# Kernel optimization log

Measured on AMD Instinct MI355X. Metric: run time of the kernel, lower is better.

## Reference

```python
import jax, jax.numpy as jnp
import numpy as np

NV, NS = 100000, 50000
DG, DS, H, OUT = 5, 6, 64, 8
EVV, EH, EIN, ESS = 1_000_000, 1_000_000, 500_000, 1_000_000


def _segsum(data, idx, n):
    return jax.ops.segment_sum(data, idx, num_segments=n)


def _edge_index(key, e, n_src, n_dst):
    k1, k2 = jax.random.split(key)
    return jnp.stack([
        jax.random.randint(k1, (e,), 0, n_src),
        jax.random.randint(k2, (e,), 0, n_dst),
    ]).astype(jnp.int64)


def setup_inputs() -> dict:
    key = jax.random.key(0)
    ks = jax.random.split(key, 16)
    s = 0.1
    inp = {
        "game_x": jax.random.normal(ks[0], (NV, DG), jnp.float32),
        "state_x": jax.random.normal(ks[1], (NS, DS), jnp.float32),
        "edge_index_v_v": _edge_index(ks[2], EVV, NV, NV),
        "edge_index_history_v_s": _edge_index(ks[3], EH, NV, NS),
        "edge_attr_history_v_s": jax.random.uniform(ks[4], (EH,), jnp.float32),
        "edge_index_in_v_s": _edge_index(ks[5], EIN, NV, NS),
        "edge_index_s_s": _edge_index(ks[6], ESS, NS, NS),
        # TAGConv(5, H, K=2): K+1 bias-free linears + bias
        "tag1_W": jax.random.normal(ks[7], (3, DG, H), jnp.float32) * s,
        "tag1_b": jnp.zeros((H,), jnp.float32),
        # TAGConv(H, H, K=3)
        "tag2_W": jax.random.normal(ks[8], (4, H, H), jnp.float32) * s,
        "tag2_b": jnp.zeros((H,), jnp.float32),
        # GraphConv((-1,-1), H): lin_rel (bias) + lin_root (no bias)
        "gc_W_rel": jax.random.normal(ks[9], (H, H), jnp.float32) * s,
        "gc_b": jnp.zeros((H,), jnp.float32),
        "gc_W_root": jax.random.normal(ks[10], (DS, H), jnp.float32) * s,
        # SAGEConv((-1,-1), H): lin_l (bias) + lin_r (no bias), mean aggr
        "sage_W_l": jax.random.normal(ks[11], (H, H), jnp.float32) * s,
        "sage_b_l": jnp.zeros((H,), jnp.float32),
        "sage_W_r": jax.random.normal(ks[12], (H, H), jnp.float32) * s,
        "lin_W": jax.random.normal(ks[13], (H, OUT), jnp.float32) * s,
        "lin_b": jnp.zeros((OUT,), jnp.float32),
    }
    return inp


def _tag_conv(x, edge_index, W, b):
    # TAGConv with gcn_norm (no self-loops): out = sum_k lin_k(A_hat^k x) + b
    n = x.shape[0]
    src, dst = edge_index[0], edge_index[1]
    deg = _segsum(jnp.ones(src.shape[0], x.dtype), dst, n)
    dinv = jnp.where(deg > 0, jax.lax.rsqrt(jnp.maximum(deg, 1e-12)), 0.0)
    norm = dinv[src] * dinv[dst]  # [E]
    out = x @ W[0]
    h = x
    for k in range(1, W.shape[0]):  # fixed, small K
        h = _segsum(h[src] * norm[:, None], dst, n)
        out = out + h @ W[k]
    return out + b


def _forward(game_x, state_x, edge_attr_history_v_s,
             tag1_W, tag1_b, tag2_W, tag2_b,
             gc_W_rel, gc_b, gc_W_root,
             sage_W_l, sage_b_l, sage_W_r, lin_W, lin_b,
             edge_index_v_v, edge_index_history_v_s,
             edge_index_in_v_s, edge_index_s_s):
    ns = state_x.shape[0]
    gx = jax.nn.relu(_tag_conv(game_x, edge_index_v_v, tag1_W, tag1_b))
    # GraphConv bipartite with edge weights: lin_rel(sum w*x_j) + lin_root(x_dst)
    src, dst = edge_index_history_v_s[0], edge_index_history_v_s[1]
    agg = _segsum(gx[src] * edge_attr_history_v_s[:, None], dst, ns)
    sx = jax.nn.relu(agg @ gc_W_rel + gc_b + state_x @ gc_W_root)
    # SAGEConv bipartite, mean aggr: lin_l(mean x_j) + lin_r(x_dst)
    src, dst = edge_index_in_v_s[0], edge_index_in_v_s[1]
    ssum = _segsum(gx[src], dst, ns)
    cnt = _segsum(jnp.ones(src.shape[0], gx.dtype), dst, ns)
    mean = ssum / jnp.maximum(cnt, 1.0)[:, None]
    sx = jax.nn.relu(mean @ sage_W_l + sage_b_l + sx @ sage_W_r)
    sx = jax.nn.relu(_tag_conv(sx, edge_index_s_s, tag2_W, tag2_b))
    return sx @ lin_W + lin_b


def reference(game_x, state_x, edge_index_v_v, edge_index_history_v_s,
              edge_attr_history_v_s, edge_index_in_v_s, edge_index_s_s,
              tag1_W, tag1_b, tag2_W, tag2_b, gc_W_rel, gc_b, gc_W_root,
              sage_W_l, sage_b_l, sage_W_r, lin_W, lin_b):
    return _forward(game_x, state_x, edge_attr_history_v_s,
                    tag1_W, tag1_b, tag2_W, tag2_b,
                    gc_W_rel, gc_b, gc_W_root,
                    sage_W_l, sage_b_l, sage_W_r, lin_W, lin_b,
                    edge_index_v_v, edge_index_history_v_s,
                    edge_index_in_v_s, edge_index_s_s)
```

## Files before the change

### kernel.cpp

```cpp
#include <hip/hip_runtime.h>

#define BLK 256
#define ACH 4096

__device__ __forceinline__ float bcast(float v, int l) {
    return __int_as_float(__builtin_amdgcn_readlane(__float_as_int(v), l));
}
__device__ __forceinline__ unsigned short f2bf(float f) {
    unsigned u = __float_as_uint(f);
    return (unsigned short)((u + 0x7FFFu + ((u >> 16) & 1u)) >> 16);
}
__device__ __forceinline__ float bf2f(unsigned short b) {
    return __uint_as_float(((unsigned)b) << 16);
}

typedef __attribute__((ext_vector_type(8))) short bf16x8;
typedef __attribute__((ext_vector_type(4))) float f32x4;

__device__ __forceinline__ void split8s(const float* p, float s, bf16x8& h, bf16x8& l) {
    #pragma unroll
    for (int j = 0; j < 8; j++) {
        float v = p[j] * s;
        unsigned short hb = f2bf(v);
        h[j] = (short)hb;
        l[j] = (short)f2bf(v - bf2f(hb));
    }
}
__device__ __forceinline__ void loadWsplit(const float* W, int kbase, int col,
                                           bf16x8& h, bf16x8& l) {
    #pragma unroll
    for (int j = 0; j < 8; j++) {
        float v = W[(size_t)(kbase + j) * 64 + col];
        unsigned short hb = f2bf(v);
        h[j] = (short)hb;
        l[j] = (short)f2bf(v - bf2f(hb));
    }
}


__global__ void k_binA1(const int* __restrict__ vd, const int* __restrict__ hd,
                        const int* __restrict__ id_, const int* __restrict__ sd,
                        int* __restrict__ Tv, int* __restrict__ Th,
                        int* __restrict__ Ti, int* __restrict__ Ts,
                        int ncv, int nch, int nci, int ncs,
                        int nbv_, int nbs_, int Ev, int Eh, int Ei, int Es) {
    __shared__ int cnt[512];
    int blk = blockIdx.x, t = threadIdx.x;
    const int* dd; int* T; int c, nc, nb, E, sf;
    if (blk < ncv)                 { dd = vd;  T = Tv; c = blk;               nc = ncv; nb = nbv_; E = Ev; sf = 8; }
    else if (blk < ncv + nch)      { dd = hd;  T = Th; c = blk - ncv;         nc = nch; nb = nbs_; E = Eh; sf = 7; }
    else if (blk < ncv + nch + nci){ dd = id_; T = Ti; c = blk - ncv - nch;   nc = nci; nb = nbs_; E = Ei; sf = 7; }
    else                           { dd = sd;  T = Ts; c = blk - ncv - nch - nci; nc = ncs; nb = nbs_; E = Es; sf = 7; }
    cnt[t] = 0; cnt[t + 256] = 0;
    __syncthreads();
    int p0 = c * ACH, p1 = min(E, p0 + ACH);
    for (int p = p0 + t; p < p1; p += 256) atomicAdd(&cnt[dd[p] >> sf], 1);
    __syncthreads();
    for (int b = t; b < nb; b += 256) T[(size_t)b * nc + c] = cnt[b];
}

__global__ void k_sb2(int* __restrict__ T, int* __restrict__ bsum,
                      int L0, int L1, int L2, int L3,
                      int nB0, int nB1, int nB2, int nB3) {
    __shared__ int sh[256];
    int blk = blockIdx.x;
    int lb, off, L;
    if (blk < nB0)                  { lb = blk;                 off = 0;            L = L0; }
    else if (blk < nB0 + nB1)       { lb = blk - nB0;           off = L0;           L = L1; }
    else if (blk < nB0 + nB1 + nB2) { lb = blk - nB0 - nB1;     off = L0 + L1;      L = L2; }
    else                            { lb = blk - nB0 - nB1 - nB2; off = L0 + L1 + L2; L = L3; }
    int i = lb * 256 + threadIdx.x;
    int v = (i < L) ? T[off + i] : 0;
    sh[threadIdx.x] = v; __syncthreads();
    for (int o2 = 1; o2 < 256; o2 <<= 1) {
        int tmp = (threadIdx.x >= o2) ? sh[threadIdx.x - o2] : 0;
        __syncthreads();
        sh[threadIdx.x] += tmp; __syncthreads();
    }
    if (i < L) T[off + i] = sh[threadIdx.x] - v;
    if (threadIdx.x == 255) bsum[blk] = sh[255];
}

__global__ void k_st2(int* __restrict__ bsum, int nB0, int nB1, int nB2, int nB3) {
    __shared__ int sh[1024];
    int g = blockIdx.x;
    int off = (g == 0) ? 0 : (g == 1) ? nB0 : (g == 2) ? nB0 + nB1 : nB0 + nB1 + nB2;
    int nb  = (g == 0) ? nB0 : (g == 1) ? nB1 : (g == 2) ? nB2 : nB3;
    int tid = threadIdx.x;
    int v = (tid < nb) ? bsum[off + tid] : 0;
    sh[tid] = v; __syncthreads();
    for (int o2 = 1; o2 < 1024; o2 <<= 1) {
        int t = (tid >= o2) ? sh[tid - o2] : 0;
        __syncthreads();
        sh[tid] += t; __syncthreads();
    }
    if (tid < nb) bsum[off + tid] = sh[tid] - v;
}

__global__ void k_sa2(int* __restrict__ T, const int* __restrict__ bsum,
                      int L0, int L1, int L2, int L3,
                      int nB0, int nB1, int nB2, int nB3) {
    int blk = blockIdx.x;
    int lb, off, L;
    if (blk < nB0)                  { lb = blk;                 off = 0;            L = L0; }
    else if (blk < nB0 + nB1)       { lb = blk - nB0;           off = L0;           L = L1; }
    else if (blk < nB0 + nB1 + nB2) { lb = blk - nB0 - nB1;     off = L0 + L1;      L = L2; }
    else                            { lb = blk - nB0 - nB1 - nB2; off = L0 + L1 + L2; L = L3; }
    int i = lb * 256 + threadIdx.x;
    if (i < L) T[off + i] += bsum[blk];
}

__global__ __launch_bounds__(512)
void k_binA2a(const int* __restrict__ vs, const int* __restrict__ vd,
              const int* __restrict__ is_, const int* __restrict__ id_,
              const int* __restrict__ ss_, const int* __restrict__ sd,
              const int* __restrict__ Tv, const int* __restrict__ Ti,
              const int* __restrict__ Ts,
              unsigned* __restrict__ vvbin, unsigned* __restrict__ inbin,
              unsigned* __restrict__ ssbin,
              int ncv, int nci, int ncs, int nbv_, int nbs_,
              int Ev, int Ei, int Es) {
    __shared__ int gbase[512], lscan[512], lcur[512];
    __shared__ unsigned sval[ACH];
    __shared__ int sdst[ACH];
    int blk = blockIdx.x, t = threadIdx.x;
    const int *srcp, *dstp, *T; unsigned* bin; int c, nc, nb, E, sf;
    if (blk < ncv)            { srcp = vs;  dstp = vd;  T = Tv; bin = vvbin; c = blk;             nc = ncv; nb = nbv_; E = Ev; sf = 8; }
    else if (blk < ncv + nci) { srcp = is_; dstp = id_; T = Ti; bin = inbin; c = blk - ncv;       nc = nci; nb = nbs_; E = Ei; sf = 7; }
    else                      { srcp = ss_; dstp = sd;  T = Ts; bin = ssbin; c = blk - ncv - nci; nc = ncs; nb = nbs_; E = Es; sf = 7; }
    int msk = (1 << sf) - 1;
    int p0 = c * ACH, p1 = min(E, p0 + ACH);
    if (t < nb) gbase[t] = T[(size_t)t * nc + c];
    lcur[t] = 0;
    int myS[8], myD[8];
    #pragma unroll
    for (int i = 0; i < 8; i++) {
        int p = p0 + t + i * 512;
        if (p < p1) { myS[i] = srcp[p]; myD[i] = dstp[p]; }
        else myD[i] = -1;
    }
    __syncthreads();
    #pragma unroll
    for (int i = 0; i < 8; i++)
        if (myD[i] >= 0) atomicAdd(&lcur[myD[i] >> sf], 1);
    __syncthreads();
    int v = lcur[t];
    lscan[t] = v;
    __syncthreads();
    for (int off = 1; off < 512; off <<= 1) {
        int tmp = (t >= off) ? lscan[t - off] : 0;
        __syncthreads();
        lscan[t] += tmp;
        __syncthreads();
    }
    int excl = lscan[t] - v;
    __syncthreads();
    lscan[t] = excl;
    lcur[t] = 0;
    __syncthreads();
    #pragma unroll
    for (int i = 0; i < 8; i++) {
        if (myD[i] < 0) continue;
        int b = myD[i] >> sf;
        int r = atomicAdd(&lcur[b], 1);
        int pos = lscan[b] + r;
        sval[pos] = ((unsigned)myS[i] << sf) | (unsigned)(myD[i] & msk);
        sdst[pos] = gbase[b] + r;
    }
    __syncthreads();
    int cntE = p1 - p0;
    for (int q = t; q < cntE; q += 512) bin[sdst[q]] = sval[q];
}

__global__ __launch_bounds__(512)
void k_binA2h(const int* __restrict__ hs, const int* __restrict__ hd,
              const float* __restrict__ hw, const int* __restrict__ Th,
              int2* __restrict__ hbin, int nch, int nbs_, int Eh) {
    __shared__ int gbase[512], lscan[512], lcur[512];
    __shared__ unsigned sval[ACH];
    __shared__ int sdst[ACH];
    __shared__ float swt[ACH];
    int c = blockIdx.x, t = threadIdx.x;
    const int sf = 7, msk = 127;
    int p0 = c * ACH, p1 = min(Eh, p0 + ACH);
    if (t < nbs_) gbase[t] = Th[(size_t)t * nch + c];
    lcur[t] = 0;
    int myS[8], myD[8]; float myW[8];
    #pragma unroll
    for (int i = 0; i < 8; i++) {
        int p = p0 + t + i * 512;
        if (p < p1) { myS[i] = hs[p]; myD[i] = hd[p]; myW[i] = hw[p]; }
        else myD[i] = -1;
    }
    __syncthreads();
    #pragma unroll
    for (int i = 0; i < 8; i++)
        if (myD[i] >= 0) atomicAdd(&lcur[myD[i] >> sf], 1);
    __syncthreads();
    int v = lcur[t];
    lscan[t] = v;
    __syncthreads();
    for (int off = 1; off < 512; off <<= 1) {
        int tmp = (t >= off) ? lscan[t - off] : 0;
        __syncthreads();
        lscan[t] += tmp;
        __syncthreads();
    }
    int excl = lscan[t] - v;
    __syncthreads();
    lscan[t] = excl;
    lcur[t] = 0;
    __syncthreads();
    #pragma unroll
    for (int i = 0; i < 8; i++) {
        if (myD[i] < 0) continue;
        int b = myD[i] >> sf;
        int r = atomicAdd(&lcur[b], 1);
        int pos = lscan[b] + r;
        sval[pos] = ((unsigned)myS[i] << sf) | (unsigned)(myD[i] & msk);
        sdst[pos] = gbase[b] + r;
        swt[pos] = myW[i];
    }
    __syncthreads();
    int cntE = p1 - p0;
    for (int q = t; q < cntE; q += 512)
        hbin[sdst[q]] = make_int2((int)sval[q], __float_as_int(swt[q]));
}

__global__ void k_binB(const unsigned* __restrict__ vvbin, const int2* __restrict__ hbin,
                       const unsigned* __restrict__ inbin, const unsigned* __restrict__ ssbin,
                       const int* __restrict__ Tv, const int* __restrict__ Th,
                       const int* __restrict__ Ti, const int* __restrict__ Ts,
                       int* __restrict__ rv, int* __restrict__ rh,
                       int* __restrict__ ri, int* __restrict__ rs,
                       float* __restrict__ dinv_v, float* __restrict__ dinv_s,
                       int* __restrict__ vvsrc, int2* __restrict__ hsw,
                       int* __restrict__ insrc, int* __restrict__ sssrc,
                       int ncv, int nch, int nci, int ncs,
                       int nbv_, int nbs_, int nv, int ns,
                       int Ev, int Eh, int Ei, int Es) {
    __shared__ int cnt[256]; __shared__ int pre[256]; __shared__ int cur[256];
    int blk = blockIdx.x, t = threadIdx.x;
    int g, b, nb, nc, sf, n, E; const int* T; int* rp;
    if (blk < nbv_)                 { g = 0; b = blk;                 nb = nbv_; nc = ncv; sf = 8; n = nv; E = Ev; T = Tv; rp = rv; }
    else if (blk < nbv_ + nbs_)     { g = 1; b = blk - nbv_;          nb = nbs_; nc = nch; sf = 7; n = ns; E = Eh; T = Th; rp = rh; }
    else if (blk < nbv_ + 2 * nbs_) { g = 2; b = blk - nbv_ - nbs_;   nb = nbs_; nc = nci; sf = 7; n = ns; E = Ei; T = Ti; rp = ri; }
    else                            { g = 3; b = blk - nbv_ - 2 * nbs_; nb = nbs_; nc = ncs; sf = 7; n = ns; E = Es; T = Ts; rp = rs; }
    int W = 1 << sf, msk = W - 1;
    int e0 = T[(size_t)b * nc];
    int e1 = (b + 1 < nb) ? T[(size_t)(b + 1) * nc] : E;
    cnt[t] = 0; __syncthreads();
    for (int p = e0 + t; p < e1; p += 256) {
        unsigned pk = (g == 1) ? (unsigned)hbin[p].x
                    : (g == 0) ? vvbin[p] : (g == 2) ? inbin[p] : ssbin[p];
        atomicAdd(&cnt[pk & msk], 1);
    }
    __syncthreads();
    int v = cnt[t];
    pre[t] = v; __syncthreads();
    for (int o2 = 1; o2 < 256; o2 <<= 1) {
        int tmp = (t >= o2) ? pre[t - o2] : 0;
        __syncthreads();
        pre[t] += tmp; __syncthreads();
    }
    int excl = pre[t] - v;
    int d = b * W + t;
    if (t < W && d < n) {
        rp[d] = e0 + excl;
        if (g == 0)      dinv_v[d] = v > 0 ? rsqrtf((float)v) : 0.f;
        else if (g == 3) dinv_s[d] = v > 0 ? rsqrtf((float)v) : 0.f;
    }
    cur[t] = e0 + excl;
    __syncthreads();
    for (int p = e0 + t; p < e1; p += 256) {
        if (g == 1) {
            int2 r = hbin[p];
            unsigned pk = (unsigned)r.x;
            int pos = atomicAdd(&cur[pk & msk], 1);
            hsw[pos] = make_int2((int)(pk >> sf), r.y);
        } else {
            unsigned pk = (g == 0) ? vvbin[p] : (g == 2) ? inbin[p] : ssbin[p];
            int pos = atomicAdd(&cur[pk & msk], 1);
            int sv = (int)(pk >> sf);
            if (g == 0)      vvsrc[pos] = sv;
            else if (g == 2) insrc[pos] = sv;
            else             sssrc[pos] = sv;
        }
    }
    if (b == 0 && t == 0) rp[n] = E;
}


__global__ void k_gather5(const float* __restrict__ x, const int* __restrict__ rowptr,
                          const int* __restrict__ csr_src, const float* __restrict__ dinv,
                          float* __restrict__ out, int n) {
    int d = blockIdx.x * blockDim.x + threadIdx.x;
    if (d >= n) return;
    int b = rowptr[d], e = rowptr[d + 1];
    float dd = dinv[d];
    float a0 = 0, a1 = 0, a2 = 0, a3 = 0, a4 = 0;
    int p = b;
    for (; p + 4 <= e; p += 4) {
        int s0 = csr_src[p], s1 = csr_src[p+1], s2 = csr_src[p+2], s3 = csr_src[p+3];
        const float* x0 = x + (size_t)s0 * 5;
        const float* x1 = x + (size_t)s1 * 5;
        const float* x2 = x + (size_t)s2 * 5;
        const float* x3 = x + (size_t)s3 * 5;
        float w0 = dd * dinv[s0], w1 = dd * dinv[s1], w2 = dd * dinv[s2], w3 = dd * dinv[s3];
        a0 += x0[0]*w0 + x1[0]*w1 + x2[0]*w2 + x3[0]*w3;
        a1 += x0[1]*w0 + x1[1]*w1 + x2[1]*w2 + x3[1]*w3;
        a2 += x0[2]*w0 + x1[2]*w1 + x2[2]*w2 + x3[2]*w3;
        a3 += x0[3]*w0 + x1[3]*w1 + x2[3]*w2 + x3[3]*w3;
        a4 += x0[4]*w0 + x1[4]*w1 + x2[4]*w2 + x3[4]*w3;
    }
    for (; p < e; p++) {
        int s = csr_src[p];
        float w = dd * dinv[s];
        const float* xp = x + (size_t)s * 5;
        a0 += xp[0]*w; a1 += xp[1]*w; a2 += xp[2]*w; a3 += xp[3]*w; a4 += xp[4]*w;
    }
    float* op = out + (size_t)d * 5;
    op[0] = a0; op[1] = a1; op[2] = a2; op[3] = a3; op[4] = a4;
}

template<int MODE, bool OUTBF>
__global__ void k_gather64(const unsigned short* __restrict__ xbf, const int* __restrict__ rowptr,
                           const int* __restrict__ csr_src, const int2* __restrict__ csr_sw,
                           const float* __restrict__ dinv, void* __restrict__ outp, int n) {
    int wid = (int)(((long long)blockIdx.x * blockDim.x + threadIdx.x) >> 6);
    if (wid >= n) return;
    int lane = threadIdx.x & 63;
    int g = lane >> 4, q = lane & 15;
    int b = rowptr[wid], e = rowptr[wid + 1];
    float dd = (MODE == 2) ? dinv[wid] : 0.f;
    float4 acc = make_float4(0.f, 0.f, 0.f, 0.f);
    int p = b + g;
    for (; p + 12 < e; p += 16) {
        int s0, s1, s2, s3;
        float w0 = 1.f, w1 = 1.f, w2 = 1.f, w3 = 1.f;
        if (MODE == 1) {
            int2 e0 = csr_sw[p], e1 = csr_sw[p+4], e2 = csr_sw[p+8], e3 = csr_sw[p+12];
            s0 = e0.x; w0 = __int_as_float(e0.y);
            s1 = e1.x; w1 = __int_as_float(e1.y);
            s2 = e2.x; w2 = __int_as_float(e2.y);
            s3 = e3.x; w3 = __int_as_float(e3.y);
        } else {
            s0 = csr_src[p]; s1 = csr_src[p+4]; s2 = csr_src[p+8]; s3 = csr_src[p+12];
            if (MODE == 2) {
                w0 = dd * dinv[s0]; w1 = dd * dinv[s1];
                w2 = dd * dinv[s2]; w3 = dd * dinv[s3];
            }
        }
        ushort4 u0 = ((const ushort4*)(xbf + (size_t)s0 * 64))[q];
        ushort4 u1 = ((const ushort4*)(xbf + (size_t)s1 * 64))[q];
        ushort4 u2 = ((const ushort4*)(xbf + (size_t)s2 * 64))[q];
        ushort4 u3 = ((const ushort4*)(xbf + (size_t)s3 * 64))[q];
        acc.x += bf2f(u0.x)*w0 + bf2f(u1.x)*w1 + bf2f(u2.x)*w2 + bf2f(u3.x)*w3;
        acc.y += bf2f(u0.y)*w0 + bf2f(u1.y)*w1 + bf2f(u2.y)*w2 + bf2f(u3.y)*w3;
        acc.z += bf2f(u0.z)*w0 + bf2f(u1.z)*w1 + bf2f(u2.z)*w2 + bf2f(u3.z)*w3;
        acc.w += bf2f(u0.w)*w0 + bf2f(u1.w)*w1 + bf2f(u2.w)*w2 + bf2f(u3.w)*w3;
    }
    for (; p < e; p += 4) {
        int s; float w = 1.f;
        if (MODE == 1) { int2 e0 = csr_sw[p]; s = e0.x; w = __int_as_float(e0.y); }
        else { s = csr_src[p]; if (MODE == 2) w = dd * dinv[s]; }
        ushort4 u = ((const ushort4*)(xbf + (size_t)s * 64))[q];
        acc.x += bf2f(u.x)*w; acc.y += bf2f(u.y)*w;
        acc.z += bf2f(u.z)*w; acc.w += bf2f(u.w)*w;
    }
    #pragma unroll
    for (int off = 16; off < 64; off <<= 1) {
        acc.x += __shfl_xor(acc.x, off, 64);
        acc.y += __shfl_xor(acc.y, off, 64);
        acc.z += __shfl_xor(acc.z, off, 64);
        acc.w += __shfl_xor(acc.w, off, 64);
    }
    if (g == 0) {
        if (OUTBF) {
            ushort4 ov;
            ov.x = f2bf(acc.x); ov.y = f2bf(acc.y); ov.z = f2bf(acc.z); ov.w = f2bf(acc.w);
            ((ushort4*)outp)[(size_t)wid * 16 + q] = ov;
        } else {
            ((float4*)outp)[(size_t)wid * 16 + q] = acc;
        }
    }
}


template<bool INIT>
__global__ __launch_bounds__(256)
void k_mm_mf(const unsigned short* __restrict__ xbf, const float* __restrict__ W,
             const float* __restrict__ bias, float* __restrict__ out, int n) {
    int wv = (int)(((long long)blockIdx.x * blockDim.x + threadIdx.x) >> 6);
    int lane = threadIdx.x & 63;
    int r0 = wv * 32;
    if (r0 >= n) return;
    int lm = lane & 15, g = lane >> 4;
    bf16x8 a[2][2];
    #pragma unroll
    for (int mt = 0; mt < 2; mt++) {
        int row = r0 + mt * 16 + lm; if (row >= n) row = n - 1;
        #pragma unroll
        for (int kh = 0; kh < 2; kh++)
            a[mt][kh] = *(const bf16x8*)(xbf + (size_t)row * 64 + kh * 32 + g * 8);
    }
    #pragma unroll
    for (int nt = 0; nt < 4; nt++) {
        int col = nt * 16 + lm;
        bf16x8 bh[2], blo[2];
        #pragma unroll
        for (int kh = 0; kh < 2; kh++) loadWsplit(W, kh * 32 + g * 8, col, bh[kh], blo[kh]);
        #pragma unroll
        for (int mt = 0; mt < 2; mt++) {
            f32x4 acc = {0.f, 0.f, 0.f, 0.f};
            #pragma unroll
            for (int kh = 0; kh < 2; kh++) {
                acc = __builtin_amdgcn_mfma_f32_16x16x32_bf16(a[mt][kh], bh[kh],  acc, 0, 0, 0);
                acc = __builtin_amdgcn_mfma_f32_16x16x32_bf16(a[mt][kh], blo[kh], acc, 0, 0, 0);
            }
            #pragma unroll
            for (int r = 0; r < 4; r++) {
                int row = r0 + mt * 16 + g * 4 + r;
                if (row < n) {
                    float base = INIT ? bias[col] : out[(size_t)row * 64 + col];
                    out[(size_t)row * 64 + col] = base + acc[r];
                }
            }
        }
    }
}

__global__ __launch_bounds__(256)
void k_sage_mf(const float* __restrict__ ssum, const int* __restrict__ rp,
               const float* __restrict__ sx, const float* __restrict__ Wl,
               const float* __restrict__ Wr, const float* __restrict__ bl,
               unsigned short* __restrict__ out, int n) {
    int wv = (int)(((long long)blockIdx.x * blockDim.x + threadIdx.x) >> 6);
    int lane = threadIdx.x & 63;
    int r0 = wv * 32;
    if (r0 >= n) return;
    int lm = lane & 15, g = lane >> 4;
    bf16x8 axh[2][2], axl[2][2], ayh[2][2], ayl[2][2];
    #pragma unroll
    for (int mt = 0; mt < 2; mt++) {
        int row = r0 + mt * 16 + lm; if (row >= n) row = n - 1;
        float cnt = (float)(rp[row + 1] - rp[row]);
        float rs = 1.f / fmaxf(cnt, 1.f);
        #pragma unroll
        for (int kh = 0; kh < 2; kh++) {
            split8s(ssum + (size_t)row * 64 + kh * 32 + g * 8, rs,  axh[mt][kh], axl[mt][kh]);
            split8s(sx   + (size_t)row * 64 + kh * 32 + g * 8, 1.f, ayh[mt][kh], ayl[mt][kh]);
        }
    }
    #pragma unroll
    for (int nt = 0; nt < 4; nt++) {
        int col = nt * 16 + lm;
        bf16x8 blh[2], bll[2], brh[2], brl[2];
        #pragma unroll
        for (int kh = 0; kh < 2; kh++) {
            loadWsplit(Wl, kh * 32 + g * 8, col, blh[kh], bll[kh]);
            loadWsplit(Wr, kh * 32 + g * 8, col, brh[kh], brl[kh]);
        }
        #pragma unroll
        for (int mt = 0; mt < 2; mt++) {
            f32x4 acc = {0.f, 0.f, 0.f, 0.f};
            #pragma unroll
            for (int kh = 0; kh < 2; kh++) {
                acc = __builtin_amdgcn_mfma_f32_16x16x32_bf16(axh[mt][kh], blh[kh], acc, 0, 0, 0);
                acc = __builtin_amdgcn_mfma_f32_16x16x32_bf16(axl[mt][kh], blh[kh], acc, 0, 0, 0);
                acc = __builtin_amdgcn_mfma_f32_16x16x32_bf16(axh[mt][kh], bll[kh], acc, 0, 0, 0);
                acc = __builtin_amdgcn_mfma_f32_16x16x32_bf16(ayh[mt][kh], brh[kh], acc, 0, 0, 0);
                acc = __builtin_amdgcn_mfma_f32_16x16x32_bf16(ayl[mt][kh], brh[kh], acc, 0, 0, 0);
                acc = __builtin_amdgcn_mfma_f32_16x16x32_bf16(ayh[mt][kh], brl[kh], acc, 0, 0, 0);
            }
            #pragma unroll
            for (int r = 0; r < 4; r++) {
                int row = r0 + mt * 16 + g * 4 + r;
                if (row < n)
                    out[(size_t)row * 64 + col] = f2bf(fmaxf(bl[col] + acc[r], 0.f));
            }
        }
    }
}

__global__ __launch_bounds__(256)
void k_gc_mf(const float* __restrict__ agg, const float* __restrict__ st,
             const float* __restrict__ Wrel, const float* __restrict__ Wroot,
             const float* __restrict__ b, float* __restrict__ out, int n) {
    int wv = (int)(((long long)blockIdx.x * blockDim.x + threadIdx.x) >> 6);
    int lane = threadIdx.x & 63;
    int r0 = wv * 32;
    if (r0 >= n) return;
    int lm = lane & 15, g = lane >> 4;
    bf16x8 axh[2][2], axl[2][2], arh[2], arl[2];
    #pragma unroll
    for (int mt = 0; mt < 2; mt++) {
        int row = r0 + mt * 16 + lm; if (row >= n) row = n - 1;
        #pragma unroll
        for (int kh = 0; kh < 2; kh++)
            split8s(agg + (size_t)row * 64 + kh * 32 + g * 8, 1.f, axh[mt][kh], axl[mt][kh]);
        #pragma unroll
        for (int j = 0; j < 8; j++) {
            int k = g * 8 + j;
            float v = (k < 6) ? st[(size_t)row * 6 + k] : 0.f;
            unsigned short hb = f2bf(v);
            arh[mt][j] = (short)hb;
            arl[mt][j] = (short)f2bf(v - bf2f(hb));
        }
    }
    #pragma unroll
    for (int nt = 0; nt < 4; nt++) {
        int col = nt * 16 + lm;
        bf16x8 bh[2], blo[2], brh, brl;
        #pragma unroll
        for (int kh = 0; kh < 2; kh++) loadWsplit(Wrel, kh * 32 + g * 8, col, bh[kh], blo[kh]);
        #pragma unroll
        for (int j = 0; j < 8; j++) {
            int k = g * 8 + j;
            float v = (k < 6) ? Wroot[(size_t)k * 64 + col] : 0.f;
            unsigned short hb = f2bf(v);
            brh[j] = (short)hb;
            brl[j] = (short)f2bf(v - bf2f(hb));
        }
        #pragma unroll
        for (int mt = 0; mt < 2; mt++) {
            f32x4 acc = {0.f, 0.f, 0.f, 0.f};
            #pragma unroll
            for (int kh = 0; kh < 2; kh++) {
                acc = __builtin_amdgcn_mfma_f32_16x16x32_bf16(axh[mt][kh], bh[kh],  acc, 0, 0, 0);
                acc = __builtin_amdgcn_mfma_f32_16x16x32_bf16(axl[mt][kh], bh[kh],  acc, 0, 0, 0);
                acc = __builtin_amdgcn_mfma_f32_16x16x32_bf16(axh[mt][kh], blo[kh], acc, 0, 0, 0);
            }
            acc = __builtin_amdgcn_mfma_f32_16x16x32_bf16(arh[mt], brh, acc, 0, 0, 0);
            acc = __builtin_amdgcn_mfma_f32_16x16x32_bf16(arl[mt], brh, acc, 0, 0, 0);
            acc = __builtin_amdgcn_mfma_f32_16x16x32_bf16(arh[mt], brl, acc, 0, 0, 0);
            #pragma unroll
            for (int r = 0; r < 4; r++) {
                int row = r0 + mt * 16 + g * 4 + r;
                if (row < n)
                    out[(size_t)row * 64 + col] = fmaxf(b[col] + acc[r], 0.f);
            }
        }
    }
}

__global__ __launch_bounds__(256, 4)
void k_tag1_w(const float* __restrict__ x, const float* __restrict__ h1,
              const float* __restrict__ h2, const float* __restrict__ W,
              const float* __restrict__ b, unsigned short* __restrict__ out, int n) {
    int wv = (int)(((long long)blockIdx.x * blockDim.x + threadIdx.x) >> 6);
    int lane = threadIdx.x & 63;
    int i0 = wv * 4;
    if (i0 >= n) return;
    float v[4], acc[4];
    #pragma unroll
    for (int r = 0; r < 4; r++) {
        int i = (i0 + r < n) ? i0 + r : n - 1;
        float t = 0.f;
        if (lane < 5)                     t = x [(size_t)i * 5 + lane];
        else if (lane >= 8 && lane < 13)  t = h1[(size_t)i * 5 + lane - 8];
        else if (lane >= 16 && lane < 21) t = h2[(size_t)i * 5 + lane - 16];
        v[r] = t;
        acc[r] = b[lane];
    }
    #pragma unroll
    for (int m = 0; m < 3; m++) {
        #pragma unroll
        for (int k = 0; k < 5; k++) {
            float wk = W[(m * 5 + k) * 64 + lane];
            #pragma unroll
            for (int r = 0; r < 4; r++) acc[r] += bcast(v[r], m * 8 + k) * wk;
        }
    }
    #pragma unroll
    for (int r = 0; r < 4; r++)
        if (i0 + r < n) out[(size_t)(i0 + r) * 64 + lane] = f2bf(fmaxf(acc[r], 0.f));
}

__global__ void k_final(const float* __restrict__ x, const float* __restrict__ W,
                        const float* __restrict__ b, float* __restrict__ out, int n) {
    int t = blockIdx.x * blockDim.x + threadIdx.x;
    if (t >= n * 8) return;
    int i = t >> 3, o = t & 7;
    float acc = b[o];
    #pragma unroll 8
    for (int k = 0; k < 64; k++) acc += fmaxf(x[i * 64 + k], 0.f) * W[k * 8 + o];
    out[t] = acc;
}

static inline unsigned gblk(long long n) { return (unsigned)((n + BLK - 1) / BLK); }
static inline unsigned gwv4(long long n) { return gblk(((n + 3) / 4) * 64); }
static inline unsigned gw32(long long n) { return gblk(((n + 31) / 32) * 64); }

extern "C" void kernel_launch(void* const* d_in, const int* in_sizes, int n_in,
                              void* d_out, int out_size, void* d_ws, size_t ws_size,
                              hipStream_t stream) {
    const float* game_x  = (const float*)d_in[0];
    const float* state_x = (const float*)d_in[1];
    const int*   ei_vv   = (const int*)d_in[2];
    const int*   ei_h    = (const int*)d_in[3];
    const float* ea_h    = (const float*)d_in[4];
    const int*   ei_in   = (const int*)d_in[5];
    const int*   ei_ss   = (const int*)d_in[6];
    const float* tag1_W  = (const float*)d_in[7];
    const float* tag1_b  = (const float*)d_in[8];
    const float* tag2_W  = (const float*)d_in[9];
    const float* tag2_b  = (const float*)d_in[10];
    const float* gc_Wrel = (const float*)d_in[11];
    const float* gc_b    = (const float*)d_in[12];
    const float* gc_Wroot= (const float*)d_in[13];
    const float* sage_Wl = (const float*)d_in[14];
    const float* sage_bl = (const float*)d_in[15];
    const float* sage_Wr = (const float*)d_in[16];
    const float* lin_W   = (const float*)d_in[17];
    const float* lin_b   = (const float*)d_in[18];

    const int NV  = in_sizes[0] / 5;
    const int NS  = in_sizes[1] / 6;
    const int EVV = in_sizes[2] / 2;
    const int EH  = in_sizes[3] / 2;
    const int EIN = in_sizes[5] / 2;
    const int ESS = in_sizes[6] / 2;

    const int *vv_s = ei_vv,  *vv_d = ei_vv + EVV;
    const int *h_s  = ei_h,   *h_d  = ei_h  + EH;
    const int *in_s = ei_in,  *in_d = ei_in + EIN;
    const int *ss_s = ei_ss,  *ss_d = ei_ss + ESS;

    const int ncv = (EVV + ACH - 1) / ACH;
    const int nch = (EH  + ACH - 1) / ACH;
    const int nci = (EIN + ACH - 1) / ACH;
    const int ncs = (ESS + ACH - 1) / ACH;
    const int nbv_ = (NV + 255) >> 8;
    const int nbs_ = (NS + 127) >> 7;
    const int Lv = nbv_ * ncv, Lh = nbs_ * nch, Li = nbs_ * nci, Ls = nbs_ * ncs;
    const int nB0 = (Lv + 255) / 256, nB1 = (Lh + 255) / 256,
              nB2 = (Li + 255) / 256, nB3 = (Ls + 255) / 256;

    float* wsf = (float*)d_ws;
    size_t o = 0;
    unsigned short* gx_bf = (unsigned short*)(wsf + o);
    float* sx3 = wsf + o; o += (size_t)NV * 32;
    float* B1 = wsf + o; o += (size_t)NS * 64;
    float* B2 = wsf + o; o += (size_t)NS * 64;
    float* B4 = wsf + o; o += (size_t)NS * 32;
    int*  vvsrc = (int*)(wsf + o); o += (size_t)EVV;
    int*  sssrc = (int*)(wsf + o); o += (size_t)ESS;
    int*  insrc = (int*)(wsf + o); o += (size_t)EIN;
    int2* hsw   = (int2*)(wsf + o); o += (size_t)EH * 2;
    int* T_all = (int*)(wsf + o); o += (size_t)(Lv + Lh + Li + Ls);
    int* bsum  = (int*)(wsf + o); o += 2048;
    int* rv = (int*)(wsf + o); o += (size_t)NV + 1;
    int* rh = (int*)(wsf + o); o += (size_t)NS + 1;
    int* ri = (int*)(wsf + o); o += (size_t)NS + 1;
    int* rs = (int*)(wsf + o); o += (size_t)NS + 1;
    float* dinv_v = wsf + o; o += (size_t)NV;
    float* dinv_s = wsf + o; o += (size_t)NS;

    int* Tv = T_all;
    int* Th = Tv + Lv;
    int* Ti = Th + Lh;
    int* Ts = Ti + Li;

    unsigned* vvbin = (unsigned*)B1;
    unsigned* inbin = vvbin + EVV;
    unsigned* ssbin = inbin + EIN;
    int2* hbin = (int2*)B2;

    unsigned short* hA_bf  = (unsigned short*)B1;
    unsigned short* hB_bf  = (unsigned short*)B2;
    unsigned short* sx2_bf = (unsigned short*)B4;

    int nbins   = nbv_ + 3 * nbs_;
    int nBtot   = nB0 + nB1 + nB2 + nB3;
    k_binA1<<<ncv + nch + nci + ncs, 256, 0, stream>>>(vv_d, h_d, in_d, ss_d, Tv, Th, Ti, Ts,
                                         ncv, nch, nci, ncs, nbv_, nbs_,
                                         EVV, EH, EIN, ESS);
    k_sb2<<<nBtot, 256, 0, stream>>>(T_all, bsum, Lv, Lh, Li, Ls, nB0, nB1, nB2, nB3);
    k_st2<<<4, 1024, 0, stream>>>(bsum, nB0, nB1, nB2, nB3);
    k_sa2<<<nBtot, 256, 0, stream>>>(T_all, bsum, Lv, Lh, Li, Ls, nB0, nB1, nB2, nB3);
    k_binA2a<<<ncv + nci + ncs, 512, 0, stream>>>(vv_s, vv_d, in_s, in_d, ss_s, ss_d,
                                                  Tv, Ti, Ts, vvbin, inbin, ssbin,
                                                  ncv, nci, ncs, nbv_, nbs_,
                                                  EVV, EIN, ESS);
    k_binA2h<<<nch, 512, 0, stream>>>(h_s, h_d, ea_h, Th, hbin, nch, nbs_, EH);
    k_binB<<<nbins, 256, 0, stream>>>(vvbin, hbin, inbin, ssbin,
                                      Tv, Th, Ti, Ts,
                                      rv, rh, ri, rs, dinv_v, dinv_s,
                                      vvsrc, hsw, insrc, sssrc,
                                      ncv, nch, nci, ncs, nbv_, nbs_,
                                      NV, NS, EVV, EH, EIN, ESS);

    float* h1v = B4;
    float* h2v = B4 + (size_t)NV * 5;
    k_gather5<<<gblk(NV), BLK, 0, stream>>>(game_x, rv, vvsrc, dinv_v, h1v, NV);
    k_gather5<<<gblk(NV), BLK, 0, stream>>>(h1v,    rv, vvsrc, dinv_v, h2v, NV);
    k_tag1_w<<<gwv4(NV), BLK, 0, stream>>>(game_x, h1v, h2v, tag1_W, tag1_b, gx_bf, NV);

    k_gather64<1, false><<<gblk((long long)NS * 64), BLK, 0, stream>>>(gx_bf, rh, nullptr, hsw, nullptr, B1, NS);
    k_gc_mf<<<gw32(NS), BLK, 0, stream>>>(B1, state_x, gc_Wrel, gc_Wroot, gc_b, B2, NS);

    k_gather64<0, false><<<gblk((long long)NS * 64), BLK, 0, stream>>>(gx_bf, ri, insrc, nullptr, nullptr, B1, NS);
    k_sage_mf<<<gw32(NS), BLK, 0, stream>>>(B1, ri, B2, sage_Wl, sage_Wr, sage_bl, sx2_bf, NS);

    k_mm_mf<true><<<gw32(NS), BLK, 0, stream>>>(sx2_bf, tag2_W, tag2_b, sx3, NS);
    k_gather64<2, true><<<gblk((long long)NS * 64), BLK, 0, stream>>>(sx2_bf, rs, sssrc, nullptr, dinv_s, hA_bf, NS);
    k_mm_mf<false><<<gw32(NS), BLK, 0, stream>>>(hA_bf, tag2_W + 4096, nullptr, sx3, NS);
    k_gather64<2, true><<<gblk((long long)NS * 64), BLK, 0, stream>>>(hA_bf, rs, sssrc, nullptr, dinv_s, hB_bf, NS);
    k_mm_mf<false><<<gw32(NS), BLK, 0, stream>>>(hB_bf, tag2_W + 8192, nullptr, sx3, NS);
    k_gather64<2, true><<<gblk((long long)NS * 64), BLK, 0, stream>>>(hB_bf, rs, sssrc, nullptr, dinv_s, hA_bf, NS);
    k_mm_mf<false><<<gw32(NS), BLK, 0, stream>>>(hA_bf, tag2_W + 12288, nullptr, sx3, NS);

    k_final<<<gblk((long long)NS * 8), BLK, 0, stream>>>(sx3, lin_W, lin_b, (float*)d_out, NS);
}
```

Measured before the change: 433.6 us.

## Fuse TAGConv2 matmuls with final linear and pack game features for gathers

Replaces the four separate per-hop MFMA matmul kernels and the final linear kernel with a single kernel. It keeps all three propagated hops in distinct buffers and computes the sum of the four linears, bias, ReLU and the output projection through LDS in one pass. This removes repeated read-modify-write traffic on the fp32 accumulator and several launches, at the cost of an extra buffer and a kernel that holds more registers. The layer-1 gathers also switch to a padded 8-float layout with dinv packed alongside x, so each neighbour costs two float4 loads instead of six scalar loads, with one extra pack kernel added.

```diff
diff --git a/kernel.cpp b/kernel.cpp
--- a/kernel.cpp
+++ b/kernel.cpp
@@ -291,36 +291,46 @@
 }
 
 
-__global__ void k_gather5(const float* __restrict__ x, const int* __restrict__ rowptr,
-                          const int* __restrict__ csr_src, const float* __restrict__ dinv,
-                          float* __restrict__ out, int n) {
+__global__ void k_pack5(const float* __restrict__ x, const float* __restrict__ dinv,
+                        float* __restrict__ P, int n) {
+    int i = blockIdx.x * blockDim.x + threadIdx.x;
+    if (i >= n) return;
+    const float* xp = x + (size_t)i * 5;
+    float4 a = make_float4(xp[0], xp[1], xp[2], xp[3]);
+    float4 b = make_float4(xp[4], dinv[i], 0.f, 0.f);
+    ((float4*)P)[(size_t)i * 2]     = a;
+    ((float4*)P)[(size_t)i * 2 + 1] = b;
+}
+
+__global__ void k_gather5p(const float* __restrict__ Pin, const int* __restrict__ rowptr,
+                           const int* __restrict__ csr_src, float* __restrict__ Pout, int n) {
     int d = blockIdx.x * blockDim.x + threadIdx.x;
     if (d >= n) return;
     int b = rowptr[d], e = rowptr[d + 1];
-    float dd = dinv[d];
+    float dd = Pin[(size_t)d * 8 + 5];
     float a0 = 0, a1 = 0, a2 = 0, a3 = 0, a4 = 0;
     int p = b;
     for (; p + 4 <= e; p += 4) {
         int s0 = csr_src[p], s1 = csr_src[p+1], s2 = csr_src[p+2], s3 = csr_src[p+3];
-        const float* x0 = x + (size_t)s0 * 5;
-        const float* x1 = x + (size_t)s1 * 5;
-        const float* x2 = x + (size_t)s2 * 5;
-        const float* x3 = x + (size_t)s3 * 5;
-        float w0 = dd * dinv[s0], w1 = dd * dinv[s1], w2 = dd * dinv[s2], w3 = dd * dinv[s3];
-        a0 += x0[0]*w0 + x1[0]*w1 + x2[0]*w2 + x3[0]*w3;
-        a1 += x0[1]*w0 + x1[1]*w1 + x2[1]*w2 + x3[1]*w3;
-        a2 += x0[2]*w0 + x1[2]*w1 + x2[2]*w2 + x3[2]*w3;
-        a3 += x0[3]*w0 + x1[3]*w1 + x2[3]*w2 + x3[3]*w3;
-        a4 += x0[4]*w0 + x1[4]*w1 + x2[4]*w2 + x3[4]*w3;
+        float4 x0a = ((const float4*)Pin)[(size_t)s0 * 2], x0b = ((const float4*)Pin)[(size_t)s0 * 2 + 1];
+        float4 x1a = ((const float4*)Pin)[(size_t)s1 * 2], x1b = ((const float4*)Pin)[(size_t)s1 * 2 + 1];
+        float4 x2a = ((const float4*)Pin)[(size_t)s2 * 2], x2b = ((const float4*)Pin)[(size_t)s2 * 2 + 1];
+        float4 x3a = ((const float4*)Pin)[(size_t)s3 * 2], x3b = ((const float4*)Pin)[(size_t)s3 * 2 + 1];
+        float w0 = dd * x0b.y, w1 = dd * x1b.y, w2 = dd * x2b.y, w3 = dd * x3b.y;
+        a0 += x0a.x*w0 + x1a.x*w1 + x2a.x*w2 + x3a.x*w3;
+        a1 += x0a.y*w0 + x1a.y*w1 + x2a.y*w2 + x3a.y*w3;
+        a2 += x0a.z*w0 + x1a.z*w1 + x2a.z*w2 + x3a.z*w3;
+        a3 += x0a.w*w0 + x1a.w*w1 + x2a.w*w2 + x3a.w*w3;
+        a4 += x0b.x*w0 + x1b.x*w1 + x2b.x*w2 + x3b.x*w3;
     }
     for (; p < e; p++) {
         int s = csr_src[p];
-        float w = dd * dinv[s];
-        const float* xp = x + (size_t)s * 5;
-        a0 += xp[0]*w; a1 += xp[1]*w; a2 += xp[2]*w; a3 += xp[3]*w; a4 += xp[4]*w;
-    }
-    float* op = out + (size_t)d * 5;
-    op[0] = a0; op[1] = a1; op[2] = a2; op[3] = a3; op[4] = a4;
+        float4 xa = ((const float4*)Pin)[(size_t)s * 2], xb = ((const float4*)Pin)[(size_t)s * 2 + 1];
+        float w = dd * xb.y;
+        a0 += xa.x*w; a1 += xa.y*w; a2 += xa.z*w; a3 += xa.w*w; a4 += xb.x*w;
+    }
+    ((float4*)Pout)[(size_t)d * 2]     = make_float4(a0, a1, a2, a3);
+    ((float4*)Pout)[(size_t)d * 2 + 1] = make_float4(a4, dd, 0.f, 0.f);
 }
 
 template<int MODE, bool OUTBF>
@@ -387,49 +397,6 @@
 }
 
 
-template<bool INIT>
-__global__ __launch_bounds__(256)
-void k_mm_mf(const unsigned short* __restrict__ xbf, const float* __restrict__ W,
-             const float* __restrict__ bias, float* __restrict__ out, int n) {
-    int wv = (int)(((long long)blockIdx.x * blockDim.x + threadIdx.x) >> 6);
-    int lane = threadIdx.x & 63;
-    int r0 = wv * 32;
-    if (r0 >= n) return;
-    int lm = lane & 15, g = lane >> 4;
-    bf16x8 a[2][2];
-    #pragma unroll
-    for (int mt = 0; mt < 2; mt++) {
-        int row = r0 + mt * 16 + lm; if (row >= n) row = n - 1;
-        #pragma unroll
-        for (int kh = 0; kh < 2; kh++)
-            a[mt][kh] = *(const bf16x8*)(xbf + (size_t)row * 64 + kh * 32 + g * 8);
-    }
-    #pragma unroll
-    for (int nt = 0; nt < 4; nt++) {
-        int col = nt * 16 + lm;
-        bf16x8 bh[2], blo[2];
-        #pragma unroll
-        for (int kh = 0; kh < 2; kh++) loadWsplit(W, kh * 32 + g * 8, col, bh[kh], blo[kh]);
-        #pragma unroll
-        for (int mt = 0; mt < 2; mt++) {
-            f32x4 acc = {0.f, 0.f, 0.f, 0.f};
-            #pragma unroll
-            for (int kh = 0; kh < 2; kh++) {
-                acc = __builtin_amdgcn_mfma_f32_16x16x32_bf16(a[mt][kh], bh[kh],  acc, 0, 0, 0);
-                acc = __builtin_amdgcn_mfma_f32_16x16x32_bf16(a[mt][kh], blo[kh], acc, 0, 0, 0);
-            }
-            #pragma unroll
-            for (int r = 0; r < 4; r++) {
-                int row = r0 + mt * 16 + g * 4 + r;
-                if (row < n) {
-                    float base = INIT ? bias[col] : out[(size_t)row * 64 + col];
-                    out[(size_t)row * 64 + col] = base + acc[r];
-                }
-            }
-        }
-    }
-}
-
 __global__ __launch_bounds__(256)
 void k_sage_mf(const float* __restrict__ ssum, const int* __restrict__ rp,
                const float* __restrict__ sx, const float* __restrict__ Wl,
@@ -544,6 +511,108 @@
     }
 }
 
+__global__ __launch_bounds__(256)
+void k_tagmm(const unsigned short* __restrict__ x0, const unsigned short* __restrict__ x1,
+             const unsigned short* __restrict__ x2, const unsigned short* __restrict__ x3,
+             const float* __restrict__ W4, const float* __restrict__ tb,
+             const float* __restrict__ lW, const float* __restrict__ lb,
+             float* __restrict__ out, int n) {
+    __shared__ float lds[4][32][64];
+    int tid = threadIdx.x;
+    int wv = (int)(((long long)blockIdx.x * blockDim.x + tid) >> 6);
+    int w = (tid >> 6) & 3;
+    int lane = tid & 63;
+    int lm = lane & 15, g = lane >> 4;
+    int r0 = wv * 32;
+    bool active = (r0 < n);
+    int r0c = active ? r0 : 0;
+    const unsigned short* xs[4] = {x0, x1, x2, x3};
+    f32x4 acc[2][4];
+    #pragma unroll
+    for (int mt = 0; mt < 2; mt++)
+        #pragma unroll
+        for (int nt = 0; nt < 4; nt++) acc[mt][nt] = (f32x4){0.f, 0.f, 0.f, 0.f};
+    #pragma unroll
+    for (int inp = 0; inp < 4; inp++) {
+        const unsigned short* xp = xs[inp];
+        const float* W = W4 + inp * 4096;
+        bf16x8 a[2][2];
+        #pragma unroll
+        for (int mt = 0; mt < 2; mt++) {
+            int row = r0c + mt * 16 + lm; if (row >= n) row = n - 1;
+            #pragma unroll
+            for (int kh = 0; kh < 2; kh++)
+                a[mt][kh] = *(const bf16x8*)(xp + (size_t)row * 64 + kh * 32 + g * 8);
+        }
+        #pragma unroll
+        for (int nt = 0; nt < 4; nt++) {
+            int col = nt * 16 + lm;
+            bf16x8 bh[2], blo[2];
+            #pragma unroll
+            for (int kh = 0; kh < 2; kh++) loadWsplit(W, kh * 32 + g * 8, col, bh[kh], blo[kh]);
+            #pragma unroll
+            for (int mt = 0; mt < 2; mt++) {
+                #pragma unroll
+                for (int kh = 0; kh < 2; kh++) {
+                    acc[mt][nt] = __builtin_amdgcn_mfma_f32_16x16x32_bf16(a[mt][kh], bh[kh],  acc[mt][nt], 0, 0, 0);
+                    acc[mt][nt] = __builtin_amdgcn_mfma_f32_16x16x32_bf16(a[mt][kh], blo[kh], acc[mt][nt], 0, 0, 0);
+                }
+            }
+        }
+    }
+    #pragma unroll
+    for (int mt = 0; mt < 2; mt++)
+        #pragma unroll
+        for (int nt = 0; nt < 4; nt++) {
+            int col = nt * 16 + lm;
+            float bias = tb[col];
+            #pragma unroll
+            for (int r = 0; r < 4; r++)
+                lds[w][mt * 16 + g * 4 + r][col] = fmaxf(bias + acc[mt][nt][r], 0.f);
+        }
+    __syncthreads();
+    bf16x8 bh2[2], bl2[2];
+    #pragma unroll
+    for (int kh = 0; kh < 2; kh++) {
+        #pragma unroll
+        for (int j = 0; j < 8; j++) {
+            int k = kh * 32 + g * 8 + j;
+            float v = (lm < 8) ? lW[k * 8 + lm] : 0.f;
+            unsigned short hb = f2bf(v);
+            bh2[kh][j] = (short)hb;
+            bl2[kh][j] = (short)f2bf(v - bf2f(hb));
+        }
+    }
+    #pragma unroll
+    for (int mt = 0; mt < 2; mt++) {
+        bf16x8 ah[2], al[2];
+        #pragma unroll
+        for (int kh = 0; kh < 2; kh++) {
+            #pragma unroll
+            for (int j = 0; j < 8; j++) {
+                float v = lds[w][mt * 16 + lm][kh * 32 + g * 8 + j];
+                unsigned short hb = f2bf(v);
+                ah[kh][j] = (short)hb;
+                al[kh][j] = (short)f2bf(v - bf2f(hb));
+            }
+        }
+        f32x4 oacc = {0.f, 0.f, 0.f, 0.f};
+        #pragma unroll
+        for (int kh = 0; kh < 2; kh++) {
+            oacc = __builtin_amdgcn_mfma_f32_16x16x32_bf16(ah[kh], bh2[kh], oacc, 0, 0, 0);
+            oacc = __builtin_amdgcn_mfma_f32_16x16x32_bf16(al[kh], bh2[kh], oacc, 0, 0, 0);
+            oacc = __builtin_amdgcn_mfma_f32_16x16x32_bf16(ah[kh], bl2[kh], oacc, 0, 0, 0);
+        }
+        if (lm < 8) {
+            #pragma unroll
+            for (int r = 0; r < 4; r++) {
+                int row = r0 + mt * 16 + g * 4 + r;
+                if (active && row < n) out[(size_t)row * 8 + lm] = oacc[r] + lb[lm];
+            }
+        }
+    }
+}
+
 __global__ __launch_bounds__(256, 4)
 void k_tag1_w(const float* __restrict__ x, const float* __restrict__ h1,
               const float* __restrict__ h2, const float* __restrict__ W,
@@ -558,8 +627,8 @@
         int i = (i0 + r < n) ? i0 + r : n - 1;
         float t = 0.f;
         if (lane < 5)                     t = x [(size_t)i * 5 + lane];
-        else if (lane >= 8 && lane < 13)  t = h1[(size_t)i * 5 + lane - 8];
-        else if (lane >= 16 && lane < 21) t = h2[(size_t)i * 5 + lane - 16];
+        else if (lane >= 8 && lane < 13)  t = h1[(size_t)i * 8 + lane - 8];
+        else if (lane >= 16 && lane < 21) t = h2[(size_t)i * 8 + lane - 16];
         v[r] = t;
         acc[r] = b[lane];
     }
@@ -575,17 +644,6 @@
     #pragma unroll
     for (int r = 0; r < 4; r++)
         if (i0 + r < n) out[(size_t)(i0 + r) * 64 + lane] = f2bf(fmaxf(acc[r], 0.f));
-}
-
-__global__ void k_final(const float* __restrict__ x, const float* __restrict__ W,
-                        const float* __restrict__ b, float* __restrict__ out, int n) {
-    int t = blockIdx.x * blockDim.x + threadIdx.x;
-    if (t >= n * 8) return;
-    int i = t >> 3, o = t & 7;
-    float acc = b[o];
-    #pragma unroll 8
-    for (int k = 0; k < 64; k++) acc += fmaxf(x[i * 64 + k], 0.f) * W[k * 8 + o];
-    out[t] = acc;
 }
 
 static inline unsigned gblk(long long n) { return (unsigned)((n + BLK - 1) / BLK); }
@@ -640,10 +698,11 @@
     float* wsf = (float*)d_ws;
     size_t o = 0;
     unsigned short* gx_bf = (unsigned short*)(wsf + o);
-    float* sx3 = wsf + o; o += (size_t)NV * 32;
+    o += (size_t)NV * 32;
     float* B1 = wsf + o; o += (size_t)NS * 64;
     float* B2 = wsf + o; o += (size_t)NS * 64;
     float* B4 = wsf + o; o += (size_t)NS * 32;
+    float* B5 = wsf + o; o += (size_t)NS * 32;
     int*  vvsrc = (int*)(wsf + o); o += (size_t)EVV;
     int*  sssrc = (int*)(wsf + o); o += (size_t)ESS;
     int*  insrc = (int*)(wsf + o); o += (size_t)EIN;
@@ -669,7 +728,11 @@
 
     unsigned short* hA_bf  = (unsigned short*)B1;
     unsigned short* hB_bf  = (unsigned short*)B2;
+    unsigned short* hC_bf  = (unsigned short*)B5;
     unsigned short* sx2_bf = (unsigned short*)B4;
+    float* P0 = B5;
+    float* H1 = B4;
+    float* H2 = B4 + (size_t)NV * 8;
 
     int nbins   = nbv_ + 3 * nbs_;
     int nBtot   = nB0 + nB1 + nB2 + nB3;
@@ -691,11 +754,10 @@
                                       ncv, nch, nci, ncs, nbv_, nbs_,
                                       NV, NS, EVV, EH, EIN, ESS);
 
-    float* h1v = B4;
-    float* h2v = B4 + (size_t)NV * 5;
-    k_gather5<<<gblk(NV), BLK, 0, stream>>>(game_x, rv, vvsrc, dinv_v, h1v, NV);
-    k_gather5<<<gblk(NV), BLK, 0, stream>>>(h1v,    rv, vvsrc, dinv_v, h2v, NV);
-    k_tag1_w<<<gwv4(NV), BLK, 0, stream>>>(game_x, h1v, h2v, tag1_W, tag1_b, gx_bf, NV);
+    k_pack5<<<gblk(NV), BLK, 0, stream>>>(game_x, dinv_v, P0, NV);
+    k_gather5p<<<gblk(NV), BLK, 0, stream>>>(P0, rv, vvsrc, H1, NV);
+    k_gather5p<<<gblk(NV), BLK, 0, stream>>>(H1, rv, vvsrc, H2, NV);
+    k_tag1_w<<<gwv4(NV), BLK, 0, stream>>>(game_x, H1, H2, tag1_W, tag1_b, gx_bf, NV);
 
     k_gather64<1, false><<<gblk((long long)NS * 64), BLK, 0, stream>>>(gx_bf, rh, nullptr, hsw, nullptr, B1, NS);
     k_gc_mf<<<gw32(NS), BLK, 0, stream>>>(B1, state_x, gc_Wrel, gc_Wroot, gc_b, B2, NS);
@@ -703,13 +765,10 @@
     k_gather64<0, false><<<gblk((long long)NS * 64), BLK, 0, stream>>>(gx_bf, ri, insrc, nullptr, nullptr, B1, NS);
     k_sage_mf<<<gw32(NS), BLK, 0, stream>>>(B1, ri, B2, sage_Wl, sage_Wr, sage_bl, sx2_bf, NS);
 
-    k_mm_mf<true><<<gw32(NS), BLK, 0, stream>>>(sx2_bf, tag2_W, tag2_b, sx3, NS);
     k_gather64<2, true><<<gblk((long long)NS * 64), BLK, 0, stream>>>(sx2_bf, rs, sssrc, nullptr, dinv_s, hA_bf, NS);
-    k_mm_mf<false><<<gw32(NS), BLK, 0, stream>>>(hA_bf, tag2_W + 4096, nullptr, sx3, NS);
     k_gather64<2, true><<<gblk((long long)NS * 64), BLK, 0, stream>>>(hA_bf, rs, sssrc, nullptr, dinv_s, hB_bf, NS);
-    k_mm_mf<false><<<gw32(NS), BLK, 0, stream>>>(hB_bf, tag2_W + 8192, nullptr, sx3, NS);
-    k_gather64<2, true><<<gblk((long long)NS * 64), BLK, 0, stream>>>(hB_bf, rs, sssrc, nullptr, dinv_s, hA_bf, NS);
-    k_mm_mf<false><<<gw32(NS), BLK, 0, stream>>>(hA_bf, tag2_W + 12288, nullptr, sx3, NS);
-
-    k_final<<<gblk((long long)NS * 8), BLK, 0, stream>>>(sx3, lin_W, lin_b, (float*)d_out, NS);
-}
+    k_gather64<2, true><<<gblk((long long)NS * 64), BLK, 0, stream>>>(hB_bf, rs, sssrc, nullptr, dinv_s, hC_bf, NS);
+    k_tagmm<<<gw32(NS), BLK, 0, stream>>>(sx2_bf, hA_bf, hB_bf, hC_bf,
+                                          tag2_W, tag2_b, lin_W, lin_b,
+                                          (float*)d_out, NS);
+}
```

After: 395.6 us. -8.8%, faster.
